# Kernel tuning notes

Measured on AMD Instinct MI355X. Metric: run time of the kernel, lower is better.

The kernel has to match this reference:

```python
import jax, jax.numpy as jnp
import numpy as np

NUM_HEADS = 8
NUM_GROUPS = 32
EPS = 1e-5


def setup_inputs() -> dict:
    key = jax.random.key(0)
    ks = jax.random.split(key, 7)
    B, C, H, W = 8, 512, 32, 32
    x = jax.random.normal(ks[0], (B, C, H, W), dtype=jnp.float32)
    # GroupNorm affine params
    gn_w = jnp.ones((C,), dtype=jnp.float32)
    gn_b = jnp.zeros((C,), dtype=jnp.float32)
    # 1x1 conv == linear over channel dim; store squeezed weights (out, in)
    qkv_w = jax.random.normal(ks[1], (3 * C, C), dtype=jnp.float32) * (1.0 / np.sqrt(C))
    qkv_b = jnp.zeros((3 * C,), dtype=jnp.float32)
    proj_w = jax.random.normal(ks[2], (C, C), dtype=jnp.float32) * (1.0 / np.sqrt(C))
    proj_b = jnp.zeros((C,), dtype=jnp.float32)
    return {"x": x, "gn_w": gn_w, "gn_b": gn_b, "qkv_w": qkv_w,
            "qkv_b": qkv_b, "proj_w": proj_w, "proj_b": proj_b}


def reference(x, gn_w, gn_b, qkv_w, qkv_b, proj_w, proj_b):
    B, C, H, W = x.shape
    G = NUM_GROUPS
    hd = C // NUM_HEADS
    scale = hd ** -0.5
    # GroupNorm: normalize over (C//G, H, W) per group
    xg = x.reshape(B, G, C // G, H, W)
    mean = xg.mean(axis=(2, 3, 4), keepdims=True)
    var = xg.var(axis=(2, 3, 4), keepdims=True)
    xn = ((xg - mean) * jax.lax.rsqrt(var + EPS)).reshape(B, C, H, W)
    xn = xn * gn_w[None, :, None, None] + gn_b[None, :, None, None]
    # QKV 1x1 conv
    qkv = jnp.einsum('bchw,oc->bohw', xn, qkv_w) + qkv_b[None, :, None, None]
    # (B, 3, heads, head_dim, HW) -> (3, B, heads, HW, head_dim)
    qkv = qkv.reshape(B, 3, NUM_HEADS, hd, H * W).transpose(1, 0, 2, 4, 3)
    q, k, v = qkv[0], qkv[1], qkv[2]
    attn = jax.nn.softmax(jnp.einsum('bhqd,bhkd->bhqk', q, k) * scale, axis=-1)
    out = jnp.einsum('bhqk,bhkd->bhqd', attn, v)  # (B, heads, HW, hd)
    out = out.transpose(0, 1, 3, 2).reshape(B, C, H, W)
    out = jnp.einsum('bchw,oc->bohw', out, proj_w) + proj_b[None, :, None, None]
    return out + x
```

## Files before the change

### kernel.cpp

```cpp
#include <hip/hip_runtime.h>
#include <hip/hip_bf16.h>
#include <math.h>

typedef __bf16 bf16_t;
typedef __bf16 bf16x8 __attribute__((ext_vector_type(8)));
typedef __bf16 bf16x4 __attribute__((ext_vector_type(4)));
typedef float  f32x4  __attribute__((ext_vector_type(4)));
typedef short  short4v __attribute__((ext_vector_type(4)));

#define NB    8
#define NC    512
#define NHW   1024
#define NHEAD 8
#define NHD   64
#define NG    32
#define NCG   16
#define NO3   1536
#define KVB   128
#define NKT   8

__device__ __forceinline__ void lds_load16(bf16_t* lds, const bf16_t* g) {
  __builtin_amdgcn_global_load_lds(
      (__attribute__((address_space(1))) unsigned int*)(g),
      (__attribute__((address_space(3))) unsigned int*)(void*)(lds),
      16, 0, 0);
}

__device__ __forceinline__ f32x4 mfma16(bf16x4 a, bf16x4 b, f32x4 c) {
#if __has_builtin(__builtin_amdgcn_mfma_f32_16x16x16bf16_1k)
  return __builtin_amdgcn_mfma_f32_16x16x16bf16_1k(
      __builtin_bit_cast(short4v, a), __builtin_bit_cast(short4v, b), c, 0, 0, 0);
#else
  f32x4 d;
  asm("v_mfma_f32_16x16x16_bf16 %0, %1, %2, %3"
      : "=v"(d) : "v"(a), "v"(b), "v"(c));
  return d;
#endif
}

__device__ __forceinline__ float fexp2(float x) {
#if __has_builtin(__builtin_amdgcn_exp2f)
  return __builtin_amdgcn_exp2f(x);
#else
  return exp2f(x);
#endif
}

__global__ __launch_bounds__(256)
void gnw_kernel(const float* __restrict__ x, const float* __restrict__ gw,
                const float* __restrict__ gb, bf16_t* __restrict__ xn,
                const float* __restrict__ qw, const float* __restrict__ pw,
                bf16_t* __restrict__ qwb, bf16_t* __restrict__ pwb)
{
  const int bid = blockIdx.x;
  const int tid = threadIdx.x;

  if (bid >= NB * NG) {
    const int gid = (bid - NB * NG) * 256 + tid;
    const int n1 = NO3 * NC / 4;
    float4 v; bf16x4 o;
    if (gid < n1) {
      v = ((const float4*)qw)[gid];
      o[0] = (bf16_t)v.x; o[1] = (bf16_t)v.y; o[2] = (bf16_t)v.z; o[3] = (bf16_t)v.w;
      ((bf16x4*)qwb)[gid] = o;
    } else {
      int g2 = gid - n1;
      v = ((const float4*)pw)[g2];
      o[0] = (bf16_t)v.x; o[1] = (bf16_t)v.y; o[2] = (bf16_t)v.z; o[3] = (bf16_t)v.w;
      ((bf16x4*)pwb)[g2] = o;
    }
    return;
  }

  const int b = bid >> 5, g = bid & 31;
  const float* xp = x + ((size_t)b * NC + g * NCG) * NHW;
  const int wave = tid >> 6, lane = tid & 63;

  float4 v[16];
  const float4* xp4 = (const float4*)xp;
  float s1 = 0.f, s2 = 0.f;
  #pragma unroll
  for (int c = 0; c < 16; ++c) {
    v[c] = xp4[c * 256 + tid];
    s1 += v[c].x + v[c].y + v[c].z + v[c].w;
    s2 += v[c].x * v[c].x + v[c].y * v[c].y + v[c].z * v[c].z + v[c].w * v[c].w;
  }
  for (int off = 32; off > 0; off >>= 1) {
    s1 += __shfl_down(s1, off);
    s2 += __shfl_down(s2, off);
  }
  __shared__ float red[16];
  if (lane == 0) { red[wave] = s1; red[8 + wave] = s2; }
  __syncthreads();
  float tot1 = red[0] + red[1] + red[2] + red[3];
  float tot2 = red[8] + red[9] + red[10] + red[11];
  const float mean = tot1 * (1.0f / 16384.0f);
  const float var  = tot2 * (1.0f / 16384.0f) - mean * mean;
  const float rstd = rsqrtf(var + 1e-5f);

  float gam[NCG], bet[NCG];
  #pragma unroll
  for (int c = 0; c < NCG; ++c) {
    gam[c] = gw[g * NCG + c] * rstd;
    bet[c] = gb[g * NCG + c] - mean * gam[c];
  }
  bf16_t* op = xn + (size_t)b * NHW * NC + g * NCG;
  #pragma unroll
  for (int jj = 0; jj < 4; ++jj) {
    int s = 4 * tid + jj;
    __align__(16) bf16_t vals[NCG];
    #pragma unroll
    for (int c = 0; c < NCG; ++c) {
      float xv = (jj == 0) ? v[c].x : (jj == 1) ? v[c].y : (jj == 2) ? v[c].z : v[c].w;
      vals[c] = (bf16_t)(xv * gam[c] + bet[c]);
    }
    *(bf16x8*)(op + (size_t)s * NC)     = *(const bf16x8*)&vals[0];
    *(bf16x8*)(op + (size_t)s * NC + 8) = *(const bf16x8*)&vals[8];
  }
}

__global__ __launch_bounds__(256, 2)
void qkv_gemm(const bf16_t* __restrict__ xn, const bf16_t* __restrict__ w,
              const float* __restrict__ bias,
              bf16_t* __restrict__ qbuf, bf16_t* __restrict__ kbuf, bf16_t* __restrict__ vbuf)
{
  __shared__ __align__(16) char smem[65536];
  const int tid = threadIdx.x;
  const int wave = tid >> 6, lane = tid & 63;
  const int quad = lane >> 4, l16 = lane & 15;
  const int wm = wave >> 1, wn = wave & 1;
  const int bid = blockIdx.x;
  const int xcd = bid & 7, slot = bid >> 3;
  const int pairIdx = xcd * 8 + slot / 12;
  const int bx = slot % 12;
  const int by = pairIdx & 7, b = pairIdx >> 3;

  const bf16_t* Ap = xn + ((size_t)b * NHW + by * 128) * NC;
  const bf16_t* Bp = w + (size_t)bx * 128 * NC;

  auto stage = [&](int k0, int bufi) {
    bf16_t* sA = (bf16_t*)(smem + bufi * 32768);
    bf16_t* sB = (bf16_t*)(smem + bufi * 32768 + 16384);
    #pragma unroll
    for (int j = 0; j < 4; ++j) {
      int c = wave * 64 + j * 256 + lane;
      int row = c >> 3, ko = ((c ^ (c >> 3)) & 7) * 8;
      lds_load16(sA + (size_t)(wave * 64 + j * 256) * 8, Ap + (size_t)row * 512 + k0 + ko);
      lds_load16(sB + (size_t)(wave * 64 + j * 256) * 8, Bp + (size_t)row * 512 + k0 + ko);
    }
  };

  f32x4 acc[4][4] = {};
  stage(0, 0);
  __syncthreads();
  const int swr = (l16 & 7) << 4;
  for (int t = 0; t < 8; ++t) {
    const int cur = t & 1;
    if (t < 7) stage((t + 1) * 64, cur ^ 1);
    const char* sA = smem + cur * 32768;
    const char* sB = sA + 16384;
    #pragma unroll
    for (int kc = 0; kc < 2; ++kc) {
      bf16x8 af[4], bfr[4];
      #pragma unroll
      for (int mi = 0; mi < 4; ++mi)
        af[mi] = *(const bf16x8*)(sA + (wm * 64 + mi * 16 + l16) * 128 + ((kc * 64 + quad * 16) ^ swr));
      #pragma unroll
      for (int ni = 0; ni < 4; ++ni)
        bfr[ni] = *(const bf16x8*)(sB + (wn * 64 + ni * 16 + l16) * 128 + ((kc * 64 + quad * 16) ^ swr));
      #pragma unroll
      for (int mi = 0; mi < 4; ++mi)
        #pragma unroll
        for (int ni = 0; ni < 4; ++ni)
          acc[mi][ni] = __builtin_amdgcn_mfma_f32_16x16x32_bf16(af[mi], bfr[ni], acc[mi][ni], 0, 0, 0);
    }
    __syncthreads();
  }

  const int obase = bx * 128 + wn * 64;
  const int sbase = by * 128 + wm * 64;
  float bv[4];
  #pragma unroll
  for (int ni = 0; ni < 4; ++ni) bv[ni] = bias[obase + ni * 16 + l16];

  if (bx < 8) {
    const bool isq = (bx < 4);
    bf16_t* basep = isq ? qbuf : kbuf;
    const float scale = isq ? 0.18033688f : 1.0f;
    #pragma unroll
    for (int ni = 0; ni < 4; ++ni) {
      int o = obase + ni * 16 + l16;
      int hh = (o >> 6) & 7, dd = o & 63;
      bf16_t* dst = basep + ((size_t)(b * NHEAD + hh) * NHW) * NHD + dd;
      #pragma unroll
      for (int mi = 0; mi < 4; ++mi)
        #pragma unroll
        for (int r = 0; r < 4; ++r) {
          int s = sbase + mi * 16 + quad * 4 + r;
          dst[(size_t)s * NHD] = (bf16_t)((acc[mi][ni][r] + bv[ni]) * scale);
        }
    }
  } else {
    bf16_t* sC = (bf16_t*)smem;
    __syncthreads();
    #pragma unroll
    for (int ni = 0; ni < 4; ++ni)
      #pragma unroll
      for (int mi = 0; mi < 4; ++mi)
        #pragma unroll
        for (int r = 0; r < 4; ++r)
          sC[(wn * 64 + ni * 16 + l16) * 136 + wm * 64 + mi * 16 + quad * 4 + r] =
              (bf16_t)(acc[mi][ni][r] + bv[ni]);
    __syncthreads();
    int o_local = tid >> 1, shalf = (tid & 1) << 6;
    int ov = (bx - 8) * 128 + o_local;
    int hh = ov >> 6, dd = ov & 63;
    bf16_t* dst = vbuf + ((size_t)(b * NHEAD + hh) * NHD + dd) * NHW + by * 128 + shalf;
    #pragma unroll
    for (int jj = 0; jj < 8; ++jj)
      *(bf16x8*)(dst + jj * 8) = *(const bf16x8*)&sC[o_local * 136 + shalf + jj * 8];
  }
}

__global__ __launch_bounds__(256, 2)
void attn_kernel(const bf16_t* __restrict__ qbuf, const bf16_t* __restrict__ kbuf,
                 const bf16_t* __restrict__ vbuf, bf16_t* __restrict__ obuf)
{
  __shared__ __align__(16) char smem[65536];
  f32x4* mO = (f32x4*)smem;
  float* mM = (float*)(smem + 16384);
  float* mL = (float*)(smem + 17408);

  const int tid = threadIdx.x;
  const int wave = tid >> 6, lane = tid & 63;
  const int quad = lane >> 4, l16 = lane & 15;
  const int wl = wave & 1;
  const int wg = wave >> 1;
  const int idx = blockIdx.x;
  const int qt = idx >> 6, h = (idx >> 3) & 7, b = idx & 7;
  const size_t bh = (size_t)b * NHEAD + h;
  const bf16_t* qp = qbuf + (bh * NHW + qt * 64 + wl * 32) * NHD;
  const char* kp = (const char*)(kbuf + bh * NHW * NHD);
  const char* vp = (const char*)(vbuf + bh * NHD * NHW);

  const int r8 = lane >> 3;
  const int swc = (((lane & 7) << 4)) ^ (r8 << 4);

  bf16x8 qf[2][2];
  #pragma unroll
  for (int stile = 0; stile < 2; ++stile)
    #pragma unroll
    for (int kc = 0; kc < 2; ++kc)
      qf[stile][kc] = *(const bf16x8*)(qp + (size_t)(stile * 16 + l16) * NHD + kc * 32 + quad * 8);

  float m_i[2] = {-1e30f, -1e30f};
  float ll[2] = {0.f, 0.f};
  f32x4 oacc[4][2] = {};

  auto stageKV = [&](int kt, char* buf) {
    #pragma unroll
    for (int j = 0; j < 4; ++j) {
      int i = wave * 4 + j;
      const char* kg = kp + ((size_t)(kt * KVB + i * 8 + r8) * NHD) * 2 + swc;
      lds_load16((bf16_t*)(buf + i * 1024), (const bf16_t*)kg);
      int dloc = i * 4 + (lane >> 4);
      int vchunk = (lane & 15) ^ (((i & 1) << 2) | (lane >> 4));
      const char* vg = vp + ((size_t)dloc * NHW + kt * KVB) * 2 + vchunk * 16;
      lds_load16((bf16_t*)(buf + 16384 + i * 1024), (const bf16_t*)vg);
    }
  };

  stageKV(0, smem);
  __syncthreads();

  const int swr = (l16 & 7) << 4;

  for (int kt = 0; kt < NKT; ++kt) {
    const int cur = kt & 1;
    const char* Kb = smem + cur * 32768;
    const char* Vb = Kb + 16384;
    if (kt < NKT - 1) stageKV(kt + 1, smem + (cur ^ 1) * 32768);

    f32x4 st[2][4];
    __builtin_amdgcn_s_setprio(1);
    #pragma unroll
    for (int mt = 0; mt < 4; ++mt) {
      const int mtg = wg * 4 + mt;
      const char* krow = Kb + (mtg * 16 + l16) * 128;
      bf16x8 ka0 = *(const bf16x8*)(krow + ((quad * 16) ^ swr));
      bf16x8 ka1 = *(const bf16x8*)(krow + ((64 + quad * 16) ^ swr));
      #pragma unroll
      for (int stile = 0; stile < 2; ++stile) {
        f32x4 z = {};
        z = __builtin_amdgcn_mfma_f32_16x16x32_bf16(ka0, qf[stile][0], z, 0, 0, 0);
        z = __builtin_amdgcn_mfma_f32_16x16x32_bf16(ka1, qf[stile][1], z, 0, 0, 0);
        st[stile][mt] = z;
      }
    }
    __builtin_amdgcn_s_setprio(0);

    #pragma unroll
    for (int stile = 0; stile < 2; ++stile) {
      float mx = st[stile][0][0];
      #pragma unroll
      for (int mt = 0; mt < 4; ++mt)
        #pragma unroll
        for (int r = 0; r < 4; ++r) mx = fmaxf(mx, st[stile][mt][r]);
      if (!__all(mx <= m_i[stile])) {
        mx = fmaxf(mx, __shfl_xor(mx, 16));
        mx = fmaxf(mx, __shfl_xor(mx, 32));
        float mnew = fmaxf(m_i[stile], mx);
        float alpha = fexp2(m_i[stile] - mnew);
        m_i[stile] = mnew;
        ll[stile] *= alpha;
        #pragma unroll
        for (int mi = 0; mi < 4; ++mi)
          #pragma unroll
          for (int r = 0; r < 4; ++r) oacc[mi][stile][r] *= alpha;
      }
      float rs = 0.f;
      #pragma unroll
      for (int mt = 0; mt < 4; ++mt)
        #pragma unroll
        for (int r = 0; r < 4; ++r) {
          float p = fexp2(st[stile][mt][r] - m_i[stile]);
          rs += p;
          st[stile][mt][r] = p;
        }
      ll[stile] += rs;
    }

    __builtin_amdgcn_s_setprio(1);
    #pragma unroll
    for (int mt = 0; mt < 4; ++mt) {
      const int mtg = wg * 4 + mt;
      bf16x4 pb[2];
      #pragma unroll
      for (int stile = 0; stile < 2; ++stile) {
        pb[stile][0] = (bf16_t)st[stile][mt][0];
        pb[stile][1] = (bf16_t)st[stile][mt][1];
        pb[stile][2] = (bf16_t)st[stile][mt][2];
        pb[stile][3] = (bf16_t)st[stile][mt][3];
      }
      const int vch = (mtg << 1) | (quad >> 1);
      const int vbo = (quad & 1) << 3;
      #pragma unroll
      for (int mi = 0; mi < 4; ++mi) {
        const char* vrow = Vb + (mi * 16 + l16) * 256;
        bf16x4 va = *(const bf16x4*)(vrow + ((vch ^ (l16 & 7)) << 4) + vbo);
        oacc[mi][0] = mfma16(va, pb[0], oacc[mi][0]);
        oacc[mi][1] = mfma16(va, pb[1], oacc[mi][1]);
      }
    }
    __builtin_amdgcn_s_setprio(0);
    __syncthreads();
  }

  float l_i[2];
  #pragma unroll
  for (int stile = 0; stile < 2; ++stile) {
    float rs = ll[stile];
    rs += __shfl_xor(rs, 16);
    rs += __shfl_xor(rs, 32);
    l_i[stile] = rs;
  }

  if (wg == 1) {
    #pragma unroll
    for (int stile = 0; stile < 2; ++stile) {
      mM[(wl * 2 + stile) * 64 + lane] = m_i[stile];
      mL[(wl * 2 + stile) * 64 + lane] = l_i[stile];
      #pragma unroll
      for (int mi = 0; mi < 4; ++mi)
        mO[((wl * 2 + stile) * 4 + mi) * 64 + lane] = oacc[mi][stile];
    }
  }
  __syncthreads();
  if (wg == 0) {
    #pragma unroll
    for (int stile = 0; stile < 2; ++stile) {
      float mB = mM[(wl * 2 + stile) * 64 + lane];
      float lB = mL[(wl * 2 + stile) * 64 + lane];
      float mS = fmaxf(m_i[stile], mB);
      float aA = fexp2(m_i[stile] - mS);
      float aB = fexp2(mB - mS);
      float inv = 1.0f / (l_i[stile] * aA + lB * aB);
      int s = qt * 64 + wl * 32 + stile * 16 + l16;
      bf16_t* orow = obuf + ((size_t)b * NHW + s) * NC + h * NHD;
      #pragma unroll
      for (int mi = 0; mi < 4; ++mi) {
        f32x4 oB = mO[((wl * 2 + stile) * 4 + mi) * 64 + lane];
        __align__(8) bf16_t o4[4];
        #pragma unroll
        for (int r = 0; r < 4; ++r)
          o4[r] = (bf16_t)((oacc[mi][stile][r] * aA + oB[r] * aB) * inv);
        *(bf16x4*)(orow + mi * 16 + quad * 4) = *(const bf16x4*)o4;
      }
    }
  }
}

__global__ __launch_bounds__(256, 2)
void proj_gemm(const bf16_t* __restrict__ ob, const bf16_t* __restrict__ w,
               const float* __restrict__ bias, const float* __restrict__ x,
               float* __restrict__ out)
{
  __shared__ __align__(16) char smem[49152];
  const int tid = threadIdx.x;
  const int wave = tid >> 6, lane = tid & 63;
  const int quad = lane >> 4, l16 = lane & 15;
  const int wm = wave & 1, wn = wave >> 1;
  const int bx = blockIdx.x, by = blockIdx.y, b = blockIdx.z;

  const bf16_t* Ap = w + (size_t)by * 64 * NC;
  const bf16_t* Bp = ob + ((size_t)b * NHW + bx * 128) * NC;

  auto stage = [&](int k0, int bufi) {
    bf16_t* sA = (bf16_t*)(smem + bufi * 24576);
    bf16_t* sB = (bf16_t*)(smem + bufi * 24576 + 8192);
    #pragma unroll
    for (int j = 0; j < 2; ++j) {
      int c = wave * 64 + j * 256 + lane;
      int row = c >> 3, ko = ((c ^ (c >> 3)) & 7) * 8;
      lds_load16(sA + (size_t)(wave * 64 + j * 256) * 8, Ap + (size_t)row * 512 + k0 + ko);
    }
    #pragma unroll
    for (int j = 0; j < 4; ++j) {
      int c = wave * 64 + j * 256 + lane;
      int row = c >> 3, ko = ((c ^ (c >> 3)) & 7) * 8;
      lds_load16(sB + (size_t)(wave * 64 + j * 256) * 8, Bp + (size_t)row * 512 + k0 + ko);
    }
  };

  f32x4 acc[2][4] = {};
  stage(0, 0);
  __syncthreads();
  const int swr = (l16 & 7) << 4;
  for (int t = 0; t < 8; ++t) {
    const int cur = t & 1;
    if (t < 7) stage((t + 1) * 64, cur ^ 1);
    const char* sA = smem + cur * 24576;
    const char* sB = sA + 8192;
    #pragma unroll
    for (int kc = 0; kc < 2; ++kc) {
      bf16x8 af[2], bfr[4];
      #pragma unroll
      for (int mi = 0; mi < 2; ++mi)
        af[mi] = *(const bf16x8*)(sA + (wm * 32 + mi * 16 + l16) * 128 + ((kc * 64 + quad * 16) ^ swr));
      #pragma unroll
      for (int ni = 0; ni < 4; ++ni)
        bfr[ni] = *(const bf16x8*)(sB + (wn * 64 + ni * 16 + l16) * 128 + ((kc * 64 + quad * 16) ^ swr));
      #pragma unroll
      for (int mi = 0; mi < 2; ++mi)
        #pragma unroll
        for (int ni = 0; ni < 4; ++ni)
          acc[mi][ni] = __builtin_amdgcn_mfma_f32_16x16x32_bf16(af[mi], bfr[ni], acc[mi][ni], 0, 0, 0);
    }
    __syncthreads();
  }

  const int cobase = by * 64 + wm * 32;
  const int sbase  = bx * 128 + wn * 64;
  #pragma unroll
  for (int mi = 0; mi < 2; ++mi)
    #pragma unroll
    for (int r = 0; r < 4; ++r) {
      int co = cobase + mi * 16 + quad * 4 + r;
      float pb = bias[co];
      const float* xrow = x + ((size_t)b * NC + co) * NHW;
      float* orow = out + ((size_t)b * NC + co) * NHW;
      #pragma unroll
      for (int ni = 0; ni < 4; ++ni) {
        int s = sbase + ni * 16 + l16;
        orow[s] = acc[mi][ni][r] + pb + xrow[s];
      }
    }
}

extern "C" void kernel_launch(void* const* d_in, const int* in_sizes, int n_in,
                              void* d_out, int out_size, void* d_ws, size_t ws_size,
                              hipStream_t stream)
{
  const float* x      = (const float*)d_in[0];
  const float* gn_w   = (const float*)d_in[1];
  const float* gn_b   = (const float*)d_in[2];
  const float* qkv_w  = (const float*)d_in[3];
  const float* qkv_b  = (const float*)d_in[4];
  const float* proj_w = (const float*)d_in[5];
  const float* proj_b = (const float*)d_in[6];
  float* out = (float*)d_out;

  char* ws = (char*)d_ws;
  bf16_t* xn   = (bf16_t*)(ws);
  bf16_t* qwb  = (bf16_t*)(ws + 8388608);
  bf16_t* pwb  = (bf16_t*)(ws + 9961472);
  bf16_t* qbuf = (bf16_t*)(ws + 10485760);
  bf16_t* kbuf = (bf16_t*)(ws + 18874368);
  bf16_t* vbuf = (bf16_t*)(ws + 27262976);
  bf16_t* obuf = xn;

  gnw_kernel<<<dim3(NB * NG + 1024), dim3(256), 0, stream>>>(
      x, gn_w, gn_b, xn, qkv_w, proj_w, qwb, pwb);
  qkv_gemm<<<dim3(768), dim3(256), 0, stream>>>(xn, qwb, qkv_b, qbuf, kbuf, vbuf);
  attn_kernel<<<dim3(1024), dim3(256), 0, stream>>>(qbuf, kbuf, vbuf, obuf);
  proj_gemm<<<dim3(8, 8, NB), dim3(256), 0, stream>>>(obuf, pwb, proj_b, x, out);
}
```

Baseline: 153.4 us.

## Process 128 queries per attention block; use plain 3D grid for QKV GEMM

Each attention block now handles two 64-query groups against the same staged K/V tiles. This doubles K/V reuse from LDS and halves the number of blocks and K/V global loads. It also doubles the per-thread accumulator and Q-fragment registers and moves the merge scratch offsets in LDS. Separately, the QKV GEMM drops its XCD-aware block-index remapping in favor of a plain 3D grid, which may change L2 locality across chiplets.

```diff
diff --git a/kernel.cpp b/kernel.cpp
--- a/kernel.cpp
+++ b/kernel.cpp
@@ -129,11 +129,7 @@
   const int wave = tid >> 6, lane = tid & 63;
   const int quad = lane >> 4, l16 = lane & 15;
   const int wm = wave >> 1, wn = wave & 1;
-  const int bid = blockIdx.x;
-  const int xcd = bid & 7, slot = bid >> 3;
-  const int pairIdx = xcd * 8 + slot / 12;
-  const int bx = slot % 12;
-  const int by = pairIdx & 7, b = pairIdx >> 3;
+  const int bx = blockIdx.x, by = blockIdx.y, b = blockIdx.z;
 
   const bf16_t* Ap = xn + ((size_t)b * NHW + by * 128) * NC;
   const bf16_t* Bp = w + (size_t)bx * 128 * NC;
@@ -228,8 +224,8 @@
 {
   __shared__ __align__(16) char smem[65536];
   f32x4* mO = (f32x4*)smem;
-  float* mM = (float*)(smem + 16384);
-  float* mL = (float*)(smem + 17408);
+  float* mM = (float*)(smem + 32768);
+  float* mL = (float*)(smem + 34816);
 
   const int tid = threadIdx.x;
   const int wave = tid >> 6, lane = tid & 63;
@@ -239,23 +235,25 @@
   const int idx = blockIdx.x;
   const int qt = idx >> 6, h = (idx >> 3) & 7, b = idx & 7;
   const size_t bh = (size_t)b * NHEAD + h;
-  const bf16_t* qp = qbuf + (bh * NHW + qt * 64 + wl * 32) * NHD;
+  const bf16_t* qp = qbuf + (bh * NHW + qt * 128 + wl * 32) * NHD;
   const char* kp = (const char*)(kbuf + bh * NHW * NHD);
   const char* vp = (const char*)(vbuf + bh * NHD * NHW);
 
   const int r8 = lane >> 3;
   const int swc = (((lane & 7) << 4)) ^ (r8 << 4);
 
-  bf16x8 qf[2][2];
-  #pragma unroll
-  for (int stile = 0; stile < 2; ++stile)
-    #pragma unroll
-    for (int kc = 0; kc < 2; ++kc)
-      qf[stile][kc] = *(const bf16x8*)(qp + (size_t)(stile * 16 + l16) * NHD + kc * 32 + quad * 8);
-
-  float m_i[2] = {-1e30f, -1e30f};
-  float ll[2] = {0.f, 0.f};
-  f32x4 oacc[4][2] = {};
+  bf16x8 qf[2][2][2];
+  #pragma unroll
+  for (int qg = 0; qg < 2; ++qg)
+    #pragma unroll
+    for (int stile = 0; stile < 2; ++stile)
+      #pragma unroll
+      for (int kc = 0; kc < 2; ++kc)
+        qf[qg][stile][kc] = *(const bf16x8*)(qp + (size_t)(qg * 64 + stile * 16 + l16) * NHD + kc * 32 + quad * 8);
+
+  float m_i[2][2] = {{-1e30f, -1e30f}, {-1e30f, -1e30f}};
+  float ll[2][2] = {};
+  f32x4 oacc[4][2][2] = {};
 
   auto stageKV = [&](int kt, char* buf) {
     #pragma unroll
@@ -281,122 +279,133 @@
     const char* Vb = Kb + 16384;
     if (kt < NKT - 1) stageKV(kt + 1, smem + (cur ^ 1) * 32768);
 
-    f32x4 st[2][4];
-    __builtin_amdgcn_s_setprio(1);
-    #pragma unroll
-    for (int mt = 0; mt < 4; ++mt) {
-      const int mtg = wg * 4 + mt;
-      const char* krow = Kb + (mtg * 16 + l16) * 128;
-      bf16x8 ka0 = *(const bf16x8*)(krow + ((quad * 16) ^ swr));
-      bf16x8 ka1 = *(const bf16x8*)(krow + ((64 + quad * 16) ^ swr));
+    #pragma unroll
+    for (int qg = 0; qg < 2; ++qg) {
+      f32x4 st[2][4];
+      __builtin_amdgcn_s_setprio(1);
+      #pragma unroll
+      for (int mt = 0; mt < 4; ++mt) {
+        const int mtg = wg * 4 + mt;
+        const char* krow = Kb + (mtg * 16 + l16) * 128;
+        bf16x8 ka0 = *(const bf16x8*)(krow + ((quad * 16) ^ swr));
+        bf16x8 ka1 = *(const bf16x8*)(krow + ((64 + quad * 16) ^ swr));
+        #pragma unroll
+        for (int stile = 0; stile < 2; ++stile) {
+          f32x4 z = {};
+          z = __builtin_amdgcn_mfma_f32_16x16x32_bf16(ka0, qf[qg][stile][0], z, 0, 0, 0);
+          z = __builtin_amdgcn_mfma_f32_16x16x32_bf16(ka1, qf[qg][stile][1], z, 0, 0, 0);
+          st[stile][mt] = z;
+        }
+      }
+      __builtin_amdgcn_s_setprio(0);
+
       #pragma unroll
       for (int stile = 0; stile < 2; ++stile) {
-        f32x4 z = {};
-        z = __builtin_amdgcn_mfma_f32_16x16x32_bf16(ka0, qf[stile][0], z, 0, 0, 0);
-        z = __builtin_amdgcn_mfma_f32_16x16x32_bf16(ka1, qf[stile][1], z, 0, 0, 0);
-        st[stile][mt] = z;
+        float mx = st[stile][0][0];
+        #pragma unroll
+        for (int mt = 0; mt < 4; ++mt)
+          #pragma unroll
+          for (int r = 0; r < 4; ++r) mx = fmaxf(mx, st[stile][mt][r]);
+        if (!__all(mx <= m_i[qg][stile])) {
+          mx = fmaxf(mx, __shfl_xor(mx, 16));
+          mx = fmaxf(mx, __shfl_xor(mx, 32));
+          float mnew = fmaxf(m_i[qg][stile], mx);
+          float alpha = fexp2(m_i[qg][stile] - mnew);
+          m_i[qg][stile] = mnew;
+          ll[qg][stile] *= alpha;
+          #pragma unroll
+          for (int mi = 0; mi < 4; ++mi)
+            #pragma unroll
+            for (int r = 0; r < 4; ++r) oacc[mi][qg][stile][r] *= alpha;
+        }
+        float rs = 0.f;
+        #pragma unroll
+        for (int mt = 0; mt < 4; ++mt)
+          #pragma unroll
+          for (int r = 0; r < 4; ++r) {
+            float p = fexp2(st[stile][mt][r] - m_i[qg][stile]);
+            rs += p;
+            st[stile][mt][r] = p;
+          }
+        ll[qg][stile] += rs;
       }
-    }
-    __builtin_amdgcn_s_setprio(0);
-
+
+      __builtin_amdgcn_s_setprio(1);
+      #pragma unroll
+      for (int mt = 0; mt < 4; ++mt) {
+        const int mtg = wg * 4 + mt;
+        bf16x4 pb[2];
+        #pragma unroll
+        for (int stile = 0; stile < 2; ++stile) {
+          pb[stile][0] = (bf16_t)st[stile][mt][0];
+          pb[stile][1] = (bf16_t)st[stile][mt][1];
+          pb[stile][2] = (bf16_t)st[stile][mt][2];
+          pb[stile][3] = (bf16_t)st[stile][mt][3];
+        }
+        const int vch = (mtg << 1) | (quad >> 1);
+        const int vbo = (quad & 1) << 3;
+        #pragma unroll
+        for (int mi = 0; mi < 4; ++mi) {
+          const char* vrow = Vb + (mi * 16 + l16) * 256;
+          bf16x4 va = *(const bf16x4*)(vrow + ((vch ^ (l16 & 7)) << 4) + vbo);
+          oacc[mi][qg][0] = mfma16(va, pb[0], oacc[mi][qg][0]);
+          oacc[mi][qg][1] = mfma16(va, pb[1], oacc[mi][qg][1]);
+        }
+      }
+      __builtin_amdgcn_s_setprio(0);
+    }
+    __syncthreads();
+  }
+
+  float l_i[2][2];
+  #pragma unroll
+  for (int qg = 0; qg < 2; ++qg)
     #pragma unroll
     for (int stile = 0; stile < 2; ++stile) {
-      float mx = st[stile][0][0];
-      #pragma unroll
-      for (int mt = 0; mt < 4; ++mt)
-        #pragma unroll
-        for (int r = 0; r < 4; ++r) mx = fmaxf(mx, st[stile][mt][r]);
-      if (!__all(mx <= m_i[stile])) {
-        mx = fmaxf(mx, __shfl_xor(mx, 16));
-        mx = fmaxf(mx, __shfl_xor(mx, 32));
-        float mnew = fmaxf(m_i[stile], mx);
-        float alpha = fexp2(m_i[stile] - mnew);
-        m_i[stile] = mnew;
-        ll[stile] *= alpha;
+      float rs = ll[qg][stile];
+      rs += __shfl_xor(rs, 16);
+      rs += __shfl_xor(rs, 32);
+      l_i[qg][stile] = rs;
+    }
+
+  if (wg == 1) {
+    #pragma unroll
+    for (int qg = 0; qg < 2; ++qg)
+      #pragma unroll
+      for (int stile = 0; stile < 2; ++stile) {
+        int rg = (qg * 2 + wl) * 2 + stile;
+        mM[rg * 64 + lane] = m_i[qg][stile];
+        mL[rg * 64 + lane] = l_i[qg][stile];
         #pragma unroll
         for (int mi = 0; mi < 4; ++mi)
-          #pragma unroll
-          for (int r = 0; r < 4; ++r) oacc[mi][stile][r] *= alpha;
+          mO[(rg * 4 + mi) * 64 + lane] = oacc[mi][qg][stile];
       }
-      float rs = 0.f;
-      #pragma unroll
-      for (int mt = 0; mt < 4; ++mt)
-        #pragma unroll
-        for (int r = 0; r < 4; ++r) {
-          float p = fexp2(st[stile][mt][r] - m_i[stile]);
-          rs += p;
-          st[stile][mt][r] = p;
-        }
-      ll[stile] += rs;
-    }
-
-    __builtin_amdgcn_s_setprio(1);
-    #pragma unroll
-    for (int mt = 0; mt < 4; ++mt) {
-      const int mtg = wg * 4 + mt;
-      bf16x4 pb[2];
-      #pragma unroll
-      for (int stile = 0; stile < 2; ++stile) {
-        pb[stile][0] = (bf16_t)st[stile][mt][0];
-        pb[stile][1] = (bf16_t)st[stile][mt][1];
-        pb[stile][2] = (bf16_t)st[stile][mt][2];
-        pb[stile][3] = (bf16_t)st[stile][mt][3];
-      }
-      const int vch = (mtg << 1) | (quad >> 1);
-      const int vbo = (quad & 1) << 3;
-      #pragma unroll
-      for (int mi = 0; mi < 4; ++mi) {
-        const char* vrow = Vb + (mi * 16 + l16) * 256;
-        bf16x4 va = *(const bf16x4*)(vrow + ((vch ^ (l16 & 7)) << 4) + vbo);
-        oacc[mi][0] = mfma16(va, pb[0], oacc[mi][0]);
-        oacc[mi][1] = mfma16(va, pb[1], oacc[mi][1]);
-      }
-    }
-    __builtin_amdgcn_s_setprio(0);
-    __syncthreads();
-  }
-
-  float l_i[2];
-  #pragma unroll
-  for (int stile = 0; stile < 2; ++stile) {
-    float rs = ll[stile];
-    rs += __shfl_xor(rs, 16);
-    rs += __shfl_xor(rs, 32);
-    l_i[stile] = rs;
-  }
-
-  if (wg == 1) {
-    #pragma unroll
-    for (int stile = 0; stile < 2; ++stile) {
-      mM[(wl * 2 + stile) * 64 + lane] = m_i[stile];
-      mL[(wl * 2 + stile) * 64 + lane] = l_i[stile];
-      #pragma unroll
-      for (int mi = 0; mi < 4; ++mi)
-        mO[((wl * 2 + stile) * 4 + mi) * 64 + lane] = oacc[mi][stile];
-    }
   }
   __syncthreads();
   if (wg == 0) {
     #pragma unroll
-    for (int stile = 0; stile < 2; ++stile) {
-      float mB = mM[(wl * 2 + stile) * 64 + lane];
-      float lB = mL[(wl * 2 + stile) * 64 + lane];
-      float mS = fmaxf(m_i[stile], mB);
-      float aA = fexp2(m_i[stile] - mS);
-      float aB = fexp2(mB - mS);
-      float inv = 1.0f / (l_i[stile] * aA + lB * aB);
-      int s = qt * 64 + wl * 32 + stile * 16 + l16;
-      bf16_t* orow = obuf + ((size_t)b * NHW + s) * NC + h * NHD;
-      #pragma unroll
-      for (int mi = 0; mi < 4; ++mi) {
-        f32x4 oB = mO[((wl * 2 + stile) * 4 + mi) * 64 + lane];
-        __align__(8) bf16_t o4[4];
-        #pragma unroll
-        for (int r = 0; r < 4; ++r)
-          o4[r] = (bf16_t)((oacc[mi][stile][r] * aA + oB[r] * aB) * inv);
-        *(bf16x4*)(orow + mi * 16 + quad * 4) = *(const bf16x4*)o4;
+    for (int qg = 0; qg < 2; ++qg)
+      #pragma unroll
+      for (int stile = 0; stile < 2; ++stile) {
+        int rg = (qg * 2 + wl) * 2 + stile;
+        float mB = mM[rg * 64 + lane];
+        float lB = mL[rg * 64 + lane];
+        float mS = fmaxf(m_i[qg][stile], mB);
+        float aA = fexp2(m_i[qg][stile] - mS);
+        float aB = fexp2(mB - mS);
+        float inv = 1.0f / (l_i[qg][stile] * aA + lB * aB);
+        int s = qt * 128 + qg * 64 + wl * 32 + stile * 16 + l16;
+        bf16_t* orow = obuf + ((size_t)b * NHW + s) * NC + h * NHD;
+        #pragma unroll
+        for (int mi = 0; mi < 4; ++mi) {
+          f32x4 oB = mO[(rg * 4 + mi) * 64 + lane];
+          __align__(8) bf16_t o4[4];
+          #pragma unroll
+          for (int r = 0; r < 4; ++r)
+            o4[r] = (bf16_t)((oacc[mi][qg][stile][r] * aA + oB[r] * aB) * inv);
+          *(bf16x4*)(orow + mi * 16 + quad * 4) = *(const bf16x4*)o4;
+        }
       }
-    }
   }
 }
 
@@ -501,7 +510,7 @@
 
   gnw_kernel<<<dim3(NB * NG + 1024), dim3(256), 0, stream>>>(
       x, gn_w, gn_b, xn, qkv_w, proj_w, qwb, pwb);
-  qkv_gemm<<<dim3(768), dim3(256), 0, stream>>>(xn, qwb, qkv_b, qbuf, kbuf, vbuf);
-  attn_kernel<<<dim3(1024), dim3(256), 0, stream>>>(qbuf, kbuf, vbuf, obuf);
+  qkv_gemm<<<dim3(12, 8, NB), dim3(256), 0, stream>>>(xn, qwb, qkv_b, qbuf, kbuf, vbuf);
+  attn_kernel<<<dim3(512), dim3(256), 0, stream>>>(qbuf, kbuf, vbuf, obuf);
   proj_gemm<<<dim3(8, 8, NB), dim3(256), 0, stream>>>(obuf, pwb, proj_b, x, out);
 }
```

Result: faster. 150.2 us (-2.1%).
